# Performance work log

Hardware: AMD Instinct MI355X
Metric: run time of the kernel (lower is better)

The kernel has to match this reference:

```python
import jax, jax.numpy as jnp
import numpy as np

B, T, E = 4, 2048, 1024
H, HS = 16, 64  # num_head, head_size; H*HS == E


def setup_inputs() -> dict:
    key = jax.random.key(0)
    ks = jax.random.split(key, 6)
    scale = 0.02
    x = jax.random.normal(ks[0], (B, T, E), dtype=jnp.float32)
    # per-head K/Q/V projection weights, stacked: [H, HS, E] (torch Linear weight layout)
    Wk = jax.random.normal(ks[1], (H, HS, E), dtype=jnp.float32) * scale
    Wq = jax.random.normal(ks[2], (H, HS, E), dtype=jnp.float32) * scale
    Wv = jax.random.normal(ks[3], (H, HS, E), dtype=jnp.float32) * scale
    Wo = jax.random.normal(ks[4], (E, E), dtype=jnp.float32) * scale  # proj weight [out, in]
    bo = jax.random.normal(ks[5], (E,), dtype=jnp.float32) * scale
    return {"x": x, "Wk": Wk, "Wq": Wq, "Wv": Wv, "Wo": Wo, "bo": bo}


def reference(x, Wk, Wq, Wv, Wo, bo):
    # per-head projections: [B,T,H,HS]
    k = jnp.einsum('bte,hde->bthd', x, Wk)
    q = jnp.einsum('bte,hde->bthd', x, Wq)
    v = jnp.einsum('bte,hde->bthd', x, Wv)
    # NOTE: source computes wei = k @ q^T (scores[t,s] = k_t . q_s), reproduced faithfully
    scores = jnp.einsum('bthd,bshd->bhts', k, q) * (HS ** -0.5)  # [B,H,T,T]
    causal = jnp.tril(jnp.ones((T, T), dtype=bool))
    scores = jnp.where(causal[None, None], scores, jnp.float32(-jnp.inf))
    wei = jax.nn.softmax(scores, axis=-1)
    out = jnp.einsum('bhts,bshd->bthd', wei, v)  # [B,T,H,HS]
    out = out.reshape(B, T, H * HS)  # concat heads (head-major order matches torch.cat)
    return out @ Wo.T + bo
```

## Files before the change

### kernel.cpp

```cpp
#include <hip/hip_runtime.h>
#include <hip/hip_bf16.h>
#include <stdint.h>

typedef __attribute__((ext_vector_type(8))) __bf16 bf16x8;
typedef __attribute__((ext_vector_type(4))) float f32x4;
typedef __attribute__((ext_vector_type(16))) float f32x16;
typedef unsigned short u16;

#define MFMA16(a, b, c) __builtin_amdgcn_mfma_f32_16x16x32_bf16((a), (b), (c), 0, 0, 0)
#define MFMA32(a, b, c) __builtin_amdgcn_mfma_f32_32x32x16_bf16((a), (b), (c), 0, 0, 0)

__device__ __forceinline__ u16 f32_to_bf16_rne(float f) {
  union { float f; uint32_t u; } v; v.f = f;
  uint32_t u = v.u;
  u += 0x7fffu + ((u >> 16) & 1u);
  return (u16)(u >> 16);
}

__device__ __forceinline__ void gl_lds16(const void* g, void* l) {
  __builtin_amdgcn_global_load_lds(
      (const __attribute__((address_space(1))) void*)(uintptr_t)g,
      (__attribute__((address_space(3))) void*)(uintptr_t)l,
      16, 0, 0);
}

__device__ __forceinline__ float fast_exp2(float x) {
#if __has_builtin(__builtin_amdgcn_exp2f)
  return __builtin_amdgcn_exp2f(x);
#else
  return exp2f(x);
#endif
}

__device__ __forceinline__ uint32_t cvt_pk_bf16(float a, float b) {
  uint32_t r;
  asm("v_cvt_pk_bf16_f32 %0, %1, %2" : "=v"(r) : "v"(a), "v"(b));
  return r;
}

__global__ void cast_all_kernel(const float* __restrict__ x, const float* __restrict__ Wk,
                                const float* __restrict__ Wq, const float* __restrict__ Wv,
                                const float* __restrict__ Wo, u16* __restrict__ xb,
                                u16* __restrict__ wqkv, u16* __restrict__ wob) {
  const int i = blockIdx.x * 256 + threadIdx.x;
  const float* src; u16* dst; int off;
  if (i < 2097152)      { src = x;  dst = xb;             off = i; }
  else if (i < 2359296) { src = Wk; dst = wqkv;           off = i - 2097152; }
  else if (i < 2621440) { src = Wq; dst = wqkv + 1048576; off = i - 2359296; }
  else if (i < 2883584) { src = Wv; dst = wqkv + 2097152; off = i - 2621440; }
  else                  { src = Wo; dst = wob;            off = i - 2883584; }
  float4 v = reinterpret_cast<const float4*>(src)[off];
  ushort4 o;
  o.x = f32_to_bf16_rne(v.x);
  o.y = f32_to_bf16_rne(v.y);
  o.z = f32_to_bf16_rne(v.z);
  o.w = f32_to_bf16_rne(v.w);
  reinterpret_cast<ushort4*>(dst)[off] = o;
}

template <int FINAL>
__global__ __launch_bounds__(256, 2) void gemm_bt_kernel(
    const u16* __restrict__ A, const u16* __restrict__ Bt,
    void* __restrict__ Cout, const float* __restrict__ bias, int M, int N, int K) {
  __shared__ __attribute__((aligned(16))) u16 As[128 * 32];
  __shared__ __attribute__((aligned(16))) u16 Bs[128 * 32];
  const int tid = threadIdx.x;
  const int lane = tid & 63;
  const int wid = tid >> 6;
  const int wr = wid >> 1, wc = wid & 1;
  const int m0 = blockIdx.y * 128, n0 = blockIdx.x * 128;

  f32x4 acc[4][4] = {};

  const int sr = lane >> 2;
  const int scc = lane & 3;
  const int sh = (sr ^ (sr >> 2)) & 3;
  const int sc = ((scc ^ sh) << 3);
  const int rl = lane & 15;
  const int rh = (rl ^ (rl >> 2)) & 3;
  const int cpr = (((lane >> 4) ^ rh) << 4);

  for (int k0 = 0; k0 < K; k0 += 32) {
    __syncthreads();
#pragma unroll
    for (int i = 0; i < 2; ++i) {
      const int c = wid * 2 + i;
      const int row = c * 16 + sr;
      gl_lds16(A + (size_t)(m0 + row) * K + k0 + sc, (char*)As + c * 1024);
      gl_lds16(Bt + (size_t)(n0 + row) * K + k0 + sc, (char*)Bs + c * 1024);
    }
    __syncthreads();

    bf16x8 af[4], bf[4];
#pragma unroll
    for (int mi = 0; mi < 4; ++mi)
      af[mi] = *(const bf16x8*)((const char*)As + (wr * 64 + mi * 16 + rl) * 64 + cpr);
#pragma unroll
    for (int ni = 0; ni < 4; ++ni)
      bf[ni] = *(const bf16x8*)((const char*)Bs + (wc * 64 + ni * 16 + rl) * 64 + cpr);
    __builtin_amdgcn_s_setprio(1);
#pragma unroll
    for (int mi = 0; mi < 4; ++mi)
#pragma unroll
      for (int ni = 0; ni < 4; ++ni)
        acc[mi][ni] = MFMA16(af[mi], bf[ni], acc[mi][ni]);
    __builtin_amdgcn_s_setprio(0);
  }

#pragma unroll
  for (int mi = 0; mi < 4; ++mi) {
#pragma unroll
    for (int ni = 0; ni < 4; ++ni) {
      const int row = m0 + wr * 64 + mi * 16 + ((lane >> 4) << 2);
      const int col = n0 + wc * 64 + ni * 16 + (lane & 15);
#pragma unroll
      for (int j = 0; j < 4; ++j) {
        if (FINAL) {
          reinterpret_cast<float*>(Cout)[(size_t)(row + j) * N + col] =
              acc[mi][ni][j] + bias[col];
        } else {
          reinterpret_cast<u16*>(Cout)[(size_t)(row + j) * N + col] =
              f32_to_bf16_rne(acc[mi][ni][j]);
        }
      }
    }
  }
}

#define KQVS 3072
#define SCL 0.18033688011f
#define NEG (-1e30f)

__device__ __forceinline__ void v_load(uint4* vr, const u16* __restrict__ Vsrc,
                                       int s0, int tid) {
#pragma unroll
  for (int it = 0; it < 2; ++it) {
    const int idx = it * 256 + tid;
    const int g = idx & 7, srow = idx >> 3;
    vr[it] = *reinterpret_cast<const uint4*>(Vsrc + (size_t)(s0 + srow) * KQVS + g * 8);
  }
}

__device__ __forceinline__ void vt_write(u16* buf, const uint4* vr, int tid) {
#pragma unroll
  for (int it = 0; it < 2; ++it) {
    const int idx = it * 256 + tid;
    const int g = idx & 7, srow = idx >> 3;
    const u16* pv = reinterpret_cast<const u16*>(&vr[it]);
#pragma unroll
    for (int u = 0; u < 8; ++u) {
      const int ue = (u + g) & 7;
      const int d = g * 8 + ue;
      buf[((srow >> 3) * 64 + d) * 8 + (srow & 7)] = pv[ue];
    }
  }
}

__global__ __launch_bounds__(256, 3) void attn_kernel(
    const u16* __restrict__ KQV, u16* __restrict__ Ob) {
  __shared__ __attribute__((aligned(16))) char smem[32768];

  const int tid = threadIdx.x;
  const int lane = tid & 63;
  const int wv = tid >> 6;
  const int l31 = lane & 31;
  const int hh = lane >> 5;
  const bool lolane = (hh == 0);

  const int idx = blockIdx.x;
  const int ttile = 15 - (idx >> 6);
  const int bhpos = idx & 63;
  const int bh = (bhpos & 7) * 8 + (bhpos >> 3);
  const int b = bh >> 4, head = bh & 15;

  const size_t rbase = (size_t)b * 2048;
  const u16* Kh = KQV + rbase * KQVS + head * 64;
  const u16* Qh = Kh + 1024;
  const u16* Vh = Kh + 2048;
  u16* Oh = Ob + rbase * 1024 + head * 64;

  const int t0 = ttile * 128;
  const int nst = 2 * ttile + 2;
  const int t0w = t0 + wv * 32;
  const int tl = t0w + l31;
  const int rb4 = 4 * hh;

#pragma unroll
  for (int i = 0; i < 4; ++i) {
    const int ch = wv * 4 + i;
    const int cc = ch >> 1;
    const int trow = (ch & 1) * 64 + lane;
    gl_lds16(Kh + (size_t)(t0 + trow) * KQVS + cc * 8, smem + 16384 + ch * 1024);
  }
#pragma unroll
  for (int i = 0; i < 2; ++i) {
    const int ch = wv * 2 + i;
    gl_lds16(Qh + (size_t)lane * KQVS + ch * 8, smem + ch * 1024);
  }
  {
    uint4 vr0[2];
    v_load(vr0, Vh, 0, tid);
    vt_write((u16*)(smem + 8192), vr0, tid);
  }
  __syncthreads();

  bf16x8 kf[4];
  {
    const u16* Ksp = (const u16*)(smem + 16384);
#pragma unroll
    for (int kk = 0; kk < 4; ++kk)
      kf[kk] = *(const bf16x8*)(Ksp + ((kk * 2 + hh) * 128 + wv * 32 + l31) * 8);
  }
  __syncthreads();

  f32x16 oa0 = {}, oa1 = {};
  float l_run = 0.f;

#pragma unroll 1
  for (int st = 0; st < nst; ++st) {
    const int cur = st & 1;
    const int s0 = st * 64;
    const bool pref = (st + 1 < nst);
    uint4 vr[2];
    if (pref) {
#pragma unroll
      for (int i = 0; i < 2; ++i) {
        const int ch = wv * 2 + i;
        gl_lds16(Qh + (size_t)(s0 + 64 + lane) * KQVS + ch * 8,
                 smem + (cur ^ 1) * 16384 + ch * 1024);
      }
      v_load(vr, Vh, s0 + 64, tid);
    }

    const bool active = (s0 <= t0w + 31);
    f32x16 sa0 = {}, sa1 = {};
    if (active) {
      const u16* qb = (const u16*)(smem + cur * 16384);
      __builtin_amdgcn_s_setprio(1);
#pragma unroll
      for (int kk = 0; kk < 4; ++kk) {
        bf16x8 a0 = *(const bf16x8*)(qb + ((kk * 2 + hh) * 64 + l31) * 8);
        bf16x8 a1 = *(const bf16x8*)(qb + ((kk * 2 + hh) * 64 + 32 + l31) * 8);
        sa0 = MFMA32(a0, kf[kk], sa0);
        sa1 = MFMA32(a1, kf[kk], sa1);
      }
      __builtin_amdgcn_s_setprio(0);

      if (s0 + 63 > t0w) {
#pragma unroll
        for (int r = 0; r < 16; ++r) {
          const int rowloc = (r & 3) + 8 * (r >> 2) + rb4;
          if (s0 + rowloc > tl) sa0[r] = NEG;
          if (s0 + 32 + rowloc > tl) sa1[r] = NEG;
        }
      }

#pragma unroll
      for (int r = 0; r < 16; ++r) {
        sa0[r] = fast_exp2(sa0[r] * SCL);
        sa1[r] = fast_exp2(sa1[r] * SCL);
      }
      float rsA = ((sa0[0] + sa0[1]) + (sa0[2] + sa0[3])) +
                  ((sa0[4] + sa0[5]) + (sa0[6] + sa0[7]));
      float rsB = ((sa0[8] + sa0[9]) + (sa0[10] + sa0[11])) +
                  ((sa0[12] + sa0[13]) + (sa0[14] + sa0[15]));
      float rsC = ((sa1[0] + sa1[1]) + (sa1[2] + sa1[3])) +
                  ((sa1[4] + sa1[5]) + (sa1[6] + sa1[7]));
      float rsD = ((sa1[8] + sa1[9]) + (sa1[10] + sa1[11])) +
                  ((sa1[12] + sa1[13]) + (sa1[14] + sa1[15]));
      float rs = (rsA + rsB) + (rsC + rsD);
      rs += __shfl_xor(rs, 32);
      l_run += rs;
    }

    if (pref) vt_write((u16*)(smem + (cur ^ 1) * 16384 + 8192), vr, tid);

    if (active) {
      const u16* vb = (const u16*)(smem + cur * 16384 + 8192);
      __builtin_amdgcn_s_setprio(1);
#define PV_WINDOW(P, r0, w)                                                   \
  {                                                                           \
    uint32_t dA = cvt_pk_bf16(P[r0 + 0], P[r0 + 1]);                          \
    uint32_t dB = cvt_pk_bf16(P[r0 + 2], P[r0 + 3]);                          \
    uint32_t dC = cvt_pk_bf16(P[r0 + 4], P[r0 + 5]);                          \
    uint32_t dD = cvt_pk_bf16(P[r0 + 6], P[r0 + 7]);                          \
    uint32_t sdA = (uint32_t)__shfl_xor((int)dA, 32);                         \
    uint32_t sdB = (uint32_t)__shfl_xor((int)dB, 32);                         \
    uint32_t sdC = (uint32_t)__shfl_xor((int)dC, 32);                         \
    uint32_t sdD = (uint32_t)__shfl_xor((int)dD, 32);                         \
    union { uint32_t u[4]; bf16x8 v; } af;                                    \
    af.u[0] = lolane ? dA : sdC;                                              \
    af.u[1] = lolane ? dB : sdD;                                              \
    af.u[2] = lolane ? sdA : dC;                                              \
    af.u[3] = lolane ? sdB : dD;                                              \
    bf16x8 bv0 = *(const bf16x8*)(vb + ((2 * (w) + hh) * 64 + l31) * 8);      \
    bf16x8 bv1 = *(const bf16x8*)(vb + ((2 * (w) + hh) * 64 + 32 + l31) * 8); \
    oa0 = MFMA32(af.v, bv0, oa0);                                             \
    oa1 = MFMA32(af.v, bv1, oa1);                                             \
  }
      PV_WINDOW(sa0, 0, 0)
      PV_WINDOW(sa0, 8, 1)
      PV_WINDOW(sa1, 0, 2)
      PV_WINDOW(sa1, 8, 3)
#undef PV_WINDOW
      __builtin_amdgcn_s_setprio(0);
    }
    __syncthreads();
  }

  {
    const float inv = 1.0f / l_run;
#pragma unroll
    for (int r = 0; r < 16; ++r) {
      const int rowloc = (r & 3) + 8 * (r >> 2) + rb4;
      const float ir = __shfl(inv, rowloc);
      const int trow = t0w + rowloc;
      Oh[(size_t)trow * 1024 + l31] = f32_to_bf16_rne(oa0[r] * ir);
      Oh[(size_t)trow * 1024 + 32 + l31] = f32_to_bf16_rne(oa1[r] * ir);
    }
  }
}

extern "C" void kernel_launch(void* const* d_in, const int* in_sizes, int n_in,
                              void* d_out, int out_size, void* d_ws, size_t ws_size,
                              hipStream_t stream) {
  (void)in_sizes; (void)n_in; (void)out_size; (void)ws_size;
  const float* x  = (const float*)d_in[0];
  const float* Wk = (const float*)d_in[1];
  const float* Wq = (const float*)d_in[2];
  const float* Wv = (const float*)d_in[3];
  const float* Wo = (const float*)d_in[4];
  const float* bo = (const float*)d_in[5];
  float* out = (float*)d_out;

  char* ws = (char*)d_ws;
  u16* xb   = (u16*)(ws);
  u16* kqv  = (u16*)(ws + ((size_t)16 << 20));
  u16* wqkv = (u16*)(ws + ((size_t)64 << 20));
  u16* wob  = (u16*)(ws + ((size_t)70 << 20));

  cast_all_kernel<<<dim3(12288), 256, 0, stream>>>(x, Wk, Wq, Wv, Wo, xb, wqkv, wob);

  gemm_bt_kernel<0><<<dim3(24, 64), 256, 0, stream>>>(xb, wqkv, kqv, nullptr, 8192, 3072, 1024);

  attn_kernel<<<dim3(1024), 256, 0, stream>>>(kqv, xb);

  gemm_bt_kernel<1><<<dim3(8, 64), 256, 0, stream>>>(xb, wob, out, bo, 8192, 1024, 1024);
}
```

Baseline: 191.1 us.

## Split long causal attention tiles across two blocks and combine partials

The eight longest causal query tiles per head are split into two key ranges handled by separate blocks. Each block writes unnormalized bf16 partial outputs and row sums, and a new combine kernel adds them and normalizes. The goal is to balance work across blocks and shorten the tail from the heaviest tiles. In exchange it adds an extra launch, extra global traffic, and an extra bf16 rounding of the partials. The combine relies on both halves sharing the same softmax reference (the kernel keeps only a running sum, apparently with no per-split max), so the partials can simply be added.

```diff
diff --git a/kernel.cpp b/kernel.cpp
--- a/kernel.cpp
+++ b/kernel.cpp
@@ -15,6 +15,11 @@
   uint32_t u = v.u;
   u += 0x7fffu + ((u >> 16) & 1u);
   return (u16)(u >> 16);
+}
+
+__device__ __forceinline__ float bf16_to_f32(u16 h) {
+  union { uint32_t u; float f; } v; v.u = ((uint32_t)h) << 16;
+  return v.f;
 }
 
 __device__ __forceinline__ void gl_lds16(const void* g, void* l) {
@@ -157,7 +162,8 @@
 }
 
 __global__ __launch_bounds__(256, 3) void attn_kernel(
-    const u16* __restrict__ KQV, u16* __restrict__ Ob) {
+    const u16* __restrict__ KQV, u16* __restrict__ Ob,
+    u16* __restrict__ pOb, float* __restrict__ pLb) {
   __shared__ __attribute__((aligned(16))) char smem[32768];
 
   const int tid = threadIdx.x;
@@ -168,9 +174,22 @@
   const bool lolane = (hh == 0);
 
   const int idx = blockIdx.x;
-  const int ttile = 15 - (idx >> 6);
-  const int bhpos = idx & 63;
-  const int bh = (bhpos & 7) * 8 + (bhpos >> 3);
+  const int virt = (idx & 7) * 192 + (idx >> 3);
+  const int bh = virt / 24;
+  const int u = virt - bh * 24;
+  int p, c, stb, ste;
+  if (u < 16) {
+    p = 15 - (u >> 1);
+    c = u & 1;
+    stb = c ? (p + 1) : 0;
+    ste = c ? (2 * p + 2) : (p + 1);
+  } else {
+    p = 23 - u;
+    c = 0;
+    stb = 0;
+    ste = 2 * p + 2;
+  }
+  const bool split = (u < 16);
   const int b = bh >> 4, head = bh & 15;
 
   const size_t rbase = (size_t)b * 2048;
@@ -179,8 +198,8 @@
   const u16* Vh = Kh + 2048;
   u16* Oh = Ob + rbase * 1024 + head * 64;
 
-  const int t0 = ttile * 128;
-  const int nst = 2 * ttile + 2;
+  const int t0 = p * 128;
+  const int nloc = ste - stb;
   const int t0w = t0 + wv * 32;
   const int tl = t0w + l31;
   const int rb4 = 4 * hh;
@@ -195,11 +214,11 @@
 #pragma unroll
   for (int i = 0; i < 2; ++i) {
     const int ch = wv * 2 + i;
-    gl_lds16(Qh + (size_t)lane * KQVS + ch * 8, smem + ch * 1024);
+    gl_lds16(Qh + (size_t)(stb * 64 + lane) * KQVS + ch * 8, smem + ch * 1024);
   }
   {
     uint4 vr0[2];
-    v_load(vr0, Vh, 0, tid);
+    v_load(vr0, Vh, stb * 64, tid);
     vt_write((u16*)(smem + 8192), vr0, tid);
   }
   __syncthreads();
@@ -217,10 +236,11 @@
   float l_run = 0.f;
 
 #pragma unroll 1
-  for (int st = 0; st < nst; ++st) {
-    const int cur = st & 1;
+  for (int j = 0; j < nloc; ++j) {
+    const int st = stb + j;
+    const int cur = j & 1;
     const int s0 = st * 64;
-    const bool pref = (st + 1 < nst);
+    const bool pref = (j + 1 < nloc);
     uint4 vr[2];
     if (pref) {
 #pragma unroll
@@ -308,7 +328,7 @@
     __syncthreads();
   }
 
-  {
+  if (!split) {
     const float inv = 1.0f / l_run;
 #pragma unroll
     for (int r = 0; r < 16; ++r) {
@@ -318,6 +338,51 @@
       Oh[(size_t)trow * 1024 + l31] = f32_to_bf16_rne(oa0[r] * ir);
       Oh[(size_t)trow * 1024 + 32 + l31] = f32_to_bf16_rne(oa1[r] * ir);
     }
+  } else {
+    const int pidx = (bh * 8 + (p - 8)) * 2 + c;
+    u16* po = pOb + (size_t)pidx * 8192;
+    float* pl = pLb + pidx * 128;
+    if (hh == 0) pl[wv * 32 + l31] = l_run;
+#pragma unroll
+    for (int r = 0; r < 16; ++r) {
+      const int rowloc = (r & 3) + 8 * (r >> 2) + rb4;
+      const int row = wv * 32 + rowloc;
+      po[row * 64 + l31] = f32_to_bf16_rne(oa0[r]);
+      po[row * 64 + 32 + l31] = f32_to_bf16_rne(oa1[r]);
+    }
+  }
+}
+
+__global__ void attn_combine_kernel(const u16* __restrict__ pOb,
+                                    const float* __restrict__ pLb,
+                                    u16* __restrict__ Ob) {
+  const int blk = blockIdx.x;
+  const int bh = blk >> 3, pi = blk & 7;
+  const int p = pi + 8;
+  const int b = bh >> 4, head = bh & 15;
+  const int base = (bh * 8 + pi) * 2;
+  const u16* po0 = pOb + (size_t)base * 8192;
+  const u16* po1 = po0 + 8192;
+  const float* pl0 = pLb + base * 128;
+  const float* pl1 = pl0 + 128;
+  u16* Oh = Ob + ((size_t)b * 2048 + p * 128) * 1024 + head * 64;
+
+  const int tid = threadIdx.x;
+  const int rr = tid >> 3;
+  const int cc = (tid & 7) * 8;
+#pragma unroll
+  for (int g = 0; g < 4; ++g) {
+    const int row = g * 32 + rr;
+    const float inv = 1.0f / (pl0[row] + pl1[row]);
+    uint4 a = *(const uint4*)(po0 + row * 64 + cc);
+    uint4 bb = *(const uint4*)(po1 + row * 64 + cc);
+    const u16* pa = (const u16*)&a;
+    const u16* pb = (const u16*)&bb;
+    u16 out[8];
+#pragma unroll
+    for (int e = 0; e < 8; ++e)
+      out[e] = f32_to_bf16_rne((bf16_to_f32(pa[e]) + bf16_to_f32(pb[e])) * inv);
+    *(uint4*)(Oh + (size_t)row * 1024 + cc) = *(const uint4*)out;
   }
 }
 
@@ -338,12 +403,15 @@
   u16* kqv  = (u16*)(ws + ((size_t)16 << 20));
   u16* wqkv = (u16*)(ws + ((size_t)64 << 20));
   u16* wob  = (u16*)(ws + ((size_t)70 << 20));
+  u16* pOb  = (u16*)(ws + ((size_t)72 << 20));
+  float* pLb = (float*)(ws + ((size_t)88 << 20));
 
   cast_all_kernel<<<dim3(12288), 256, 0, stream>>>(x, Wk, Wq, Wv, Wo, xb, wqkv, wob);
 
   gemm_bt_kernel<0><<<dim3(24, 64), 256, 0, stream>>>(xb, wqkv, kqv, nullptr, 8192, 3072, 1024);
 
-  attn_kernel<<<dim3(1024), 256, 0, stream>>>(kqv, xb);
+  attn_kernel<<<dim3(1536), 256, 0, stream>>>(kqv, xb, pOb, pLb);
+  attn_combine_kernel<<<dim3(512), 256, 0, stream>>>(pOb, pLb, xb);
 
   gemm_bt_kernel<1><<<dim3(8, 64), 256, 0, stream>>>(xb, wob, out, bo, 8192, 1024, 1024);
 }
```

Result: slower. 217.6 us (+13.9%).
